# Kernel optimization log

Measured on AMD Instinct MI355X. Metric: run time of the kernel, lower is better.

The kernel has to match this reference:

```python
import jax, jax.numpy as jnp
import numpy as np

CODEBOOK_SIZE = 8192
TOKEN_SIZE = 256
COMMITMENT_COST = 0.25
B, C, H, W = 32, 256, 32, 32


def setup_inputs() -> dict:
    key = jax.random.key(0)
    k1, k2 = jax.random.split(key)
    z = jax.random.normal(k1, (B, C, H, W), dtype=jnp.float32)
    # torch init: uniform_(-1/codebook_size, 1/codebook_size)
    embedding = jax.random.uniform(
        k2, (CODEBOOK_SIZE, TOKEN_SIZE), dtype=jnp.float32,
        minval=-1.0 / CODEBOOK_SIZE, maxval=1.0 / CODEBOOK_SIZE)
    return {"z": z, "embedding": embedding}


def reference(z, embedding):
    # b c h w -> b h w c
    z = jnp.transpose(z.astype(jnp.float32), (0, 2, 3, 1))
    b, h, w, c = z.shape
    z_flat = z.reshape(-1, c)  # [N, c]

    # squared euclidean distances: ||z||^2 + ||e||^2 - 2 z e^T
    d = (jnp.sum(z_flat ** 2, axis=1, keepdims=True)
         + jnp.sum(embedding ** 2, axis=1)
         - 2.0 * jnp.einsum('nd,kd->nk', z_flat, embedding))  # [N, K]
    idx = jnp.argmin(d, axis=1)  # [N]

    z_q = embedding[idx].reshape(z.shape)  # [b,h,w,c]

    commitment_loss = COMMITMENT_COST * jnp.mean(
        (jax.lax.stop_gradient(z_q) - z) ** 2)
    codebook_loss = jnp.mean((z_q - jax.lax.stop_gradient(z)) ** 2)
    loss = commitment_loss + codebook_loss

    # straight-through estimator
    z_q_st = z + jax.lax.stop_gradient(z_q - z)
    z_q_out = jnp.transpose(z_q_st, (0, 3, 1, 2))  # b h w c -> b c h w

    min_encoding_indices = idx.reshape(b, h, w)
    return (z_q_out, loss, commitment_loss, codebook_loss,
            min_encoding_indices)
```

## Files before the change

kernel.cpp:

```cpp
#include <hip/hip_runtime.h>
#include <float.h>

#define NBATCH 32
#define NCHAN  256
#define NHW    1024
#define NTOK   32768
#define NK     8192
#define ND     256
#define ZELEMS 8388608
#define OUT_LOSS 8388608
#define OUT_IDX  8388611
#define MARGIN   1.2e-4f

typedef short bf16x8  __attribute__((ext_vector_type(8)));
typedef float f32x4   __attribute__((ext_vector_type(4)));
typedef float f32x16  __attribute__((ext_vector_type(16)));

__device__ __forceinline__ unsigned short f2bf(float f) {
    unsigned int u = __float_as_uint(f);
    u += 0x7FFFu + ((u >> 16) & 1u);
    return (unsigned short)(u >> 16);
}

__device__ __forceinline__ float embed8(float x, int code) {
    return __int_as_float((__float_as_int(x) & 0xFFFFFF00) | code);
}


__global__ __launch_bounds__(256) void k_cast(const float* __restrict__ zg,
                                              const float* __restrict__ E,
                                              unsigned short* __restrict__ Epre,
                                              unsigned short* __restrict__ Zpre,
                                              float* __restrict__ en,
                                              double* __restrict__ acc,
                                              int* __restrict__ counter) {
    __shared__ unsigned short buf[128][34];
    const int t = threadIdx.x;
    if (blockIdx.x < 1024) {
        int g = blockIdx.x * 256 + t;
        int code = g >> 5, c16 = g & 31;
        int kc = c16 >> 2, ks = (c16 >> 1) & 1, lhi = c16 & 1;
        const float4* E4 = (const float4*)(E + code * ND + c16 * 8);
        float4 a = E4[0], b = E4[1];
        float s = a.x*a.x + a.y*a.y + a.z*a.z + a.w*a.w
                + b.x*b.x + b.y*b.y + b.z*b.z + b.w*b.w;
        #pragma unroll
        for (int off = 1; off < 32; off <<= 1) s += __shfl_xor(s, off, 64);
        if ((t & 31) == 0) en[code] = s;
        unsigned int u[4];
        u[0] = (unsigned int)f2bf(a.x) | ((unsigned int)f2bf(a.y) << 16);
        u[1] = (unsigned int)f2bf(a.z) | ((unsigned int)f2bf(a.w) << 16);
        u[2] = (unsigned int)f2bf(b.x) | ((unsigned int)f2bf(b.y) << 16);
        u[3] = (unsigned int)f2bf(b.z) | ((unsigned int)f2bf(b.w) << 16);
        *(uint4*)((char*)Epre + (size_t)(code >> 7) * 65536 + kc * 8192
                  + (ks * 2 + lhi) * 2048 + (code & 127) * 16) =
            make_uint4(u[0], u[1], u[2], u[3]);
        if (blockIdx.x == 0 && t == 0) { acc[0] = 0.0; counter[0] = 0; }
    } else {
        int bi = blockIdx.x - 1024;
        int b = bi >> 6, kc = (bi >> 3) & 7, hwt = bi & 7;
        int c0 = kc * 32, hw0 = hwt * 128;
        #pragma unroll
        for (int r = 0; r < 4; ++r) {
            int idx = r * 256 + t;
            int c = idx >> 5, q = idx & 31;
            float4 v = *(const float4*)&zg[(b * 256 + c0 + c) * 1024 + hw0 + q * 4];
            buf[q * 4 + 0][c] = f2bf(v.x);
            buf[q * 4 + 1][c] = f2bf(v.y);
            buf[q * 4 + 2][c] = f2bf(v.z);
            buf[q * 4 + 3][c] = f2bf(v.w);
        }
        __syncthreads();
        int tok = t >> 1, ks = t & 1;
        char* base = (char*)Zpre + (size_t)((b * 8 + hwt) * 8 + kc) * 8192;
        #pragma unroll
        for (int lhi = 0; lhi < 2; ++lhi) {
            unsigned int u[4];
            #pragma unroll
            for (int k = 0; k < 4; ++k) {
                int cc = ks * 16 + lhi * 8 + 2 * k;
                u[k] = (unsigned int)buf[tok][cc] | ((unsigned int)buf[tok][cc + 1] << 16);
            }
            *(uint4*)(base + (ks * 2 + lhi) * 2048 + tok * 16) =
                make_uint4(u[0], u[1], u[2], u[3]);
        }
    }
}

__global__ __launch_bounds__(256, 2) void k_dist(const unsigned short* __restrict__ Epre,
                                                 const unsigned short* __restrict__ Zpre,
                                                 const float* __restrict__ en,
                                                 float2* __restrict__ part2) {
    __shared__ __align__(16) char Elds[3][16384];
    __shared__ __align__(16) char Zlds[3][8192];
    __shared__ float2 red[2][128];
    __shared__ float en_s[256];

    const int t    = threadIdx.x;
    const int kbb2 = blockIdx.x;
    const int mb   = blockIdx.y;
    const int n0   = mb * 128;
    const int w    = t >> 6, lane = t & 63;
    const int l31  = lane & 31, lhi = lane >> 5;
    const int wm   = w >> 1, wn = w & 1;

    const char* Esrc = (const char*)Epre + (size_t)kbb2 * 131072;
    const char* Zsrc = (const char*)Zpre + (size_t)mb * 65536;

    auto STAGE = [&](int bb, int kc) {
        #pragma unroll
        for (int s2 = 0; s2 < 2; ++s2)
            #pragma unroll
            for (int h = 0; h < 2; ++h)
                __builtin_amdgcn_global_load_lds(
                    (const unsigned int*)(Esrc + (size_t)s2 * 65536 + kc * 8192 + h * 4096 + t * 16),
                    (unsigned int*)&Elds[bb][s2 * 8192 + h * 4096 + t * 16], 16, 0, 0);
        #pragma unroll
        for (int h = 0; h < 2; ++h)
            __builtin_amdgcn_global_load_lds(
                (const unsigned int*)(Zsrc + kc * 8192 + h * 4096 + t * 16),
                (unsigned int*)&Zlds[bb][h * 4096 + t * 16], 16, 0, 0);
    };

    f32x16 acc[4][2];
    #pragma unroll
    for (int i = 0; i < 4; ++i)
        #pragma unroll
        for (int j = 0; j < 2; ++j) acc[i][j] = (f32x16)0.0f;

    float en_v = en[kbb2 * 256 + t];
    STAGE(0, 0);
    STAGE(1, 1);
    asm volatile("s_waitcnt vmcnt(6)" ::: "memory");
    __builtin_amdgcn_s_barrier();

    const int eoff = wm * 8192 + lhi * 2048 + l31 * 16;
    const int zoff = lhi * 2048 + (wn * 64 + l31) * 16;

    #pragma unroll
    for (int kc = 0; kc < 8; ++kc) {
        const int pp = kc % 3;
        const char* Eb = &Elds[pp][0] + eoff;
        const char* Zb = &Zlds[pp][0] + zoff;
        bf16x8 ea[4][2], zb[2][2];
        #pragma unroll
        for (int i = 0; i < 4; ++i)
            #pragma unroll
            for (int ks = 0; ks < 2; ++ks)
                ea[i][ks] = *(const bf16x8*)(Eb + ks * 4096 + i * 512);
        #pragma unroll
        for (int j = 0; j < 2; ++j)
            #pragma unroll
            for (int ks = 0; ks < 2; ++ks)
                zb[j][ks] = *(const bf16x8*)(Zb + ks * 4096 + j * 512);
        asm volatile("s_waitcnt lgkmcnt(0)" ::: "memory");
        __builtin_amdgcn_s_barrier();
        __builtin_amdgcn_sched_barrier(0);
        if (kc < 6) STAGE((kc + 2) % 3, kc + 2);

        __builtin_amdgcn_s_setprio(1);
        #pragma unroll
        for (int ks = 0; ks < 2; ++ks)
            #pragma unroll
            for (int i = 0; i < 4; ++i)
                #pragma unroll
                for (int j = 0; j < 2; ++j)
                    acc[i][j] = __builtin_amdgcn_mfma_f32_32x32x16_bf16(
                        ea[i][ks], zb[j][ks], acc[i][j], 0, 0, 0);
        __builtin_amdgcn_s_setprio(0);
        if (kc < 6)      { asm volatile("s_waitcnt vmcnt(6)" ::: "memory"); __builtin_amdgcn_s_barrier(); }
        else if (kc == 6){ asm volatile("s_waitcnt vmcnt(0)" ::: "memory"); __builtin_amdgcn_s_barrier(); }
    }

    en_s[t] = en_v;
    __syncthreads();

    float v1[2][4], v2[2][4];
    #pragma unroll
    for (int j = 0; j < 2; ++j)
        #pragma unroll
        for (int i = 0; i < 4; ++i) { v1[j][i] = FLT_MAX; v2[j][i] = FLT_MAX; }
    #pragma unroll
    for (int i = 0; i < 4; ++i) {
        const int cb = wm * 128 + i * 32 + lhi * 4;
        #pragma unroll
        for (int rq = 0; rq < 4; ++rq) {
            f32x4 ev = *(const f32x4*)&en_s[cb + 8 * rq];
            #pragma unroll
            for (int rr = 0; rr < 4; ++rr) {
                const int r = rq * 4 + rr;
                const int code = cb + 8 * rq + rr;
                #pragma unroll
                for (int j = 0; j < 2; ++j) {
                    float s  = fmaf(-2.0f, acc[i][j][r], ev[rr]);
                    float se = embed8(s, code);
                    v2[j][i] = __builtin_amdgcn_fmed3f(se, v1[j][i], v2[j][i]);
                    v1[j][i] = fminf(v1[j][i], se);
                }
            }
        }
    }
    float m1[2], m2[2];
    #pragma unroll
    for (int j = 0; j < 2; ++j) {
        float a1 = fminf(v1[j][0], v1[j][1]);
        float ah = fmaxf(v1[j][0], v1[j][1]);
        float a2 = fminf(ah, fminf(v2[j][0], v2[j][1]));
        float b1 = fminf(v1[j][2], v1[j][3]);
        float bh = fmaxf(v1[j][2], v1[j][3]);
        float b2 = fminf(bh, fminf(v2[j][2], v2[j][3]));
        m1[j] = fminf(a1, b1);
        m2[j] = fminf(fmaxf(a1, b1), fminf(a2, b2));
    }
    #pragma unroll
    for (int j = 0; j < 2; ++j) {
        float b1 = __shfl_xor(m1[j], 32, 64);
        float b2 = __shfl_xor(m2[j], 32, 64);
        float hi = fmaxf(m1[j], b1);
        m1[j] = fminf(m1[j], b1);
        m2[j] = fminf(fminf(hi, m2[j]), b2);
    }
    if (lane < 32) {
        #pragma unroll
        for (int j = 0; j < 2; ++j)
            red[wm][wn * 64 + j * 32 + l31] = make_float2(m1[j], m2[j]);
    }
    __syncthreads();
    if (t < 128) {
        float2 A = red[0][t], B = red[1][t];
        float g1 = fminf(A.x, B.x);
        float g2 = fminf(fminf(fmaxf(A.x, B.x), A.y), B.y);
        part2[(size_t)kbb2 * NTOK + n0 + t] = make_float2(g1, g2);
    }
}

__global__ __launch_bounds__(256) void k_refine(const float* __restrict__ zg,
                                                const float* __restrict__ E,
                                                const float* __restrict__ en,
                                                const float2* __restrict__ part2,
                                                int* __restrict__ idxw,
                                                float* __restrict__ outF,
                                                double* __restrict__ acc,
                                                int* __restrict__ counter) {
    __shared__ float Zs[256 * 65];
    __shared__ double lred[4];
    const int t = threadIdx.x;
    const int n0 = blockIdx.x * 64;
    const int b = n0 >> 10, hw0 = n0 & 1023;

    #pragma unroll
    for (int r = 0; r < 16; ++r) {
        int li = r * 256 + t;
        int c = li >> 4, q = li & 15;
        float4 v = *(const float4*)&zg[(b * 256 + c) * 1024 + hw0 + q * 4];
        Zs[c * 65 + q * 4 + 0] = v.x;
        Zs[c * 65 + q * 4 + 1] = v.y;
        Zs[c * 65 + q * 4 + 2] = v.z;
        Zs[c * 65 + q * 4 + 3] = v.w;
    }
    __syncthreads();

    const int w = t >> 6, l = t & 63;
    double lsum = 0.0;
    for (int it = 0; it < 16; ++it) {
        const int tokl = w * 16 + it;
        const int n = n0 + tokl;

        float zreg[4];
        #pragma unroll
        for (int j = 0; j < 4; ++j) zreg[j] = Zs[(64 * j + l) * 65 + tokl];

        double z2 = 0.0;
        #pragma unroll
        for (int j = 0; j < 4; ++j) z2 += (double)zreg[j] * (double)zreg[j];
        #pragma unroll
        for (int m = 1; m < 64; m <<= 1) z2 += __shfl_xor(z2, m, 64);
        const float z2f = (float)z2;

        float2 p = make_float2(FLT_MAX, FLT_MAX);
        if (l < 32) p = part2[(size_t)l * NTOK + n];
        int code1 = (l << 8) | (__float_as_int(p.x) & 0xFF);
        int code2 = (l << 8) | (__float_as_int(p.y) & 0xFF);

        float vmin = p.x;
        #pragma unroll
        for (int m = 1; m < 64; m <<= 1) vmin = fminf(vmin, __shfl_xor(vmin, m, 64));
        const float thr = vmin + MARGIN;

        unsigned long long m1 = __ballot(p.x <= thr);
        unsigned long long m2 = __ballot(p.y <= thr);

        float bdq = FLT_MAX; int bidx = 0x7fffffff; double gw = 0.0;
        #pragma unroll
        for (int pass = 0; pass < 2; ++pass) {
            unsigned long long mm = pass ? m2 : m1;
            int ibits = pass ? code2 : code1;
            while (mm) {
                int src = __ffsll(mm) - 1; mm &= mm - 1;
                int cidx = __shfl(ibits, src, 64);
                const float* erow = E + cidx * ND;
                double g = (double)zreg[0] * (double)erow[l]
                         + (double)zreg[1] * (double)erow[64 + l]
                         + (double)zreg[2] * (double)erow[128 + l]
                         + (double)zreg[3] * (double)erow[192 + l];
                #pragma unroll
                for (int mk = 1; mk < 64; mk <<= 1) g += __shfl_xor(g, mk, 64);
                float c  = (float)(2.0 * g);
                float dq = z2f - c;
                if (dq < bdq || (dq == bdq && cidx < bidx)) { bdq = dq; bidx = cidx; gw = g; }
            }
        }
        if (l == 0) {
            idxw[n] = bidx; outF[OUT_IDX + n] = (float)bidx;
            lsum += (double)en[bidx] - 2.0 * gw + z2;
        }
    }
    if (l == 0) lred[w] = lsum;
    __syncthreads();
    if (t == 0) {
        atomicAdd(acc, lred[0] + lred[1] + lred[2] + lred[3]);
        __threadfence();
        int old = atomicAdd(counter, 1);
        if (old == 511) {
            double total = atomicAdd(acc, 0.0);
            double mse = total / 8388608.0;
            outF[OUT_LOSS + 0] = (float)(1.25 * mse);
            outF[OUT_LOSS + 1] = (float)(0.25 * mse);
            outF[OUT_LOSS + 2] = (float)mse;
        }
    }
}

__global__ __launch_bounds__(256) void k_gather(const float* __restrict__ E,
                                                const int* __restrict__ idxw,
                                                float* __restrict__ out) {
    __shared__ __align__(16) float Es[64 * 256];
    __shared__ int sidx[64];
    const int t = threadIdx.x;
    const int b = blockIdx.x >> 4, ht = blockIdx.x & 15;

    if (t < 64) sidx[t] = idxw[b * 1024 + ht * 64 + t];
    __syncthreads();
    const float4* E4 = (const float4*)E;
    #pragma unroll
    for (int r = 0; r < 16; ++r) {
        int li = r * 256 + t;
        int row = li >> 6, slot = li & 63;
        float4 v = E4[(size_t)sidx[row] * 64 + slot];
        *(float4*)&Es[row * 256 + ((slot ^ (row & 15)) * 4)] = v;
    }
    __syncthreads();

    const int hw = t & 63, wv = t >> 6;
    #pragma unroll 8
    for (int cc = 0; cc < 64; ++cc) {
        int c = wv * 64 + cc;
        float e = Es[hw * 256 + (((c >> 2) ^ (hw & 15)) * 4) + (c & 3)];
        size_t gi = (size_t)(b * 256 + c) * 1024 + ht * 64 + hw;
        out[gi] = e;
    }
}

extern "C" void kernel_launch(void* const* d_in, const int* in_sizes, int n_in,
                              void* d_out, int out_size, void* d_ws, size_t ws_size,
                              hipStream_t stream) {
    const float* zg = (const float*)d_in[0];
    const float* E  = (const float*)d_in[1];
    float* out = (float*)d_out;
    float* wsf = (float*)d_ws;
    double* acc     = (double*)wsf;
    int*    counter = (int*)(wsf + 2);
    float*  en      = wsf + 64;
    int*    idxw    = (int*)(wsf + 64 + NK);
    float2* part2   = (float2*)(wsf + 64 + NK + NTOK);
    unsigned short* Epre = (unsigned short*)(wsf + 64 + NK + NTOK + 4194304);
    unsigned short* Zpre = (unsigned short*)d_out;

    k_cast  <<<3072, 256, 0, stream>>>(zg, E, Epre, Zpre, en, acc, counter);
    k_dist  <<<dim3(32, 256), 256, 0, stream>>>(Epre, Zpre, en, part2);
    k_refine<<<NTOK / 64, 256, 0, stream>>>(zg, E, en, part2, idxw, out, acc, counter);
    k_gather<<<512, 256, 0, stream>>>(E, idxw, out);
}
```

Before: 282.1 us.

## Load Z operand directly into double-buffered registers instead of LDS staging

```diff
diff --git a/kernel.cpp b/kernel.cpp
--- a/kernel.cpp
+++ b/kernel.cpp
@@ -92,7 +92,6 @@
                                                  const float* __restrict__ en,
                                                  float2* __restrict__ part2) {
     __shared__ __align__(16) char Elds[3][16384];
-    __shared__ __align__(16) char Zlds[3][8192];
     __shared__ float2 red[2][128];
     __shared__ float en_s[256];
 
@@ -107,7 +106,7 @@
     const char* Esrc = (const char*)Epre + (size_t)kbb2 * 131072;
     const char* Zsrc = (const char*)Zpre + (size_t)mb * 65536;
 
-    auto STAGE = [&](int bb, int kc) {
+    auto STAGE_E = [&](int bb, int kc) {
         #pragma unroll
         for (int s2 = 0; s2 < 2; ++s2)
             #pragma unroll
@@ -115,13 +114,19 @@
                 __builtin_amdgcn_global_load_lds(
                     (const unsigned int*)(Esrc + (size_t)s2 * 65536 + kc * 8192 + h * 4096 + t * 16),
                     (unsigned int*)&Elds[bb][s2 * 8192 + h * 4096 + t * 16], 16, 0, 0);
-        #pragma unroll
-        for (int h = 0; h < 2; ++h)
-            __builtin_amdgcn_global_load_lds(
-                (const unsigned int*)(Zsrc + kc * 8192 + h * 4096 + t * 16),
-                (unsigned int*)&Zlds[bb][h * 4096 + t * 16], 16, 0, 0);
     };
 
+    bf16x8 zbR[2][2][2];
+    const char* Zp = Zsrc + lhi * 2048 + (wn * 64 + l31) * 16;
+    auto LOADZ = [&](int set, int kc) {
+        const char* p = Zp + kc * 8192;
+        #pragma unroll
+        for (int j = 0; j < 2; ++j)
+            #pragma unroll
+            for (int ks = 0; ks < 2; ++ks)
+                zbR[set][j][ks] = *(const bf16x8*)(p + ks * 4096 + j * 512);
+    };
+
     f32x16 acc[4][2];
     #pragma unroll
     for (int i = 0; i < 4; ++i)
@@ -129,34 +134,30 @@
         for (int j = 0; j < 2; ++j) acc[i][j] = (f32x16)0.0f;
 
     float en_v = en[kbb2 * 256 + t];
-    STAGE(0, 0);
-    STAGE(1, 1);
-    asm volatile("s_waitcnt vmcnt(6)" ::: "memory");
+    LOADZ(0, 0);
+    STAGE_E(0, 0);
+    STAGE_E(1, 1);
+    asm volatile("s_waitcnt vmcnt(4)" ::: "memory");
     __builtin_amdgcn_s_barrier();
 
     const int eoff = wm * 8192 + lhi * 2048 + l31 * 16;
-    const int zoff = lhi * 2048 + (wn * 64 + l31) * 16;
 
     #pragma unroll
     for (int kc = 0; kc < 8; ++kc) {
-        const int pp = kc % 3;
-        const char* Eb = &Elds[pp][0] + eoff;
-        const char* Zb = &Zlds[pp][0] + zoff;
-        bf16x8 ea[4][2], zb[2][2];
+        const int eb = kc % 3, zs = kc & 1;
+        const char* Eb = &Elds[eb][0] + eoff;
+        bf16x8 ea[4][2];
         #pragma unroll
         for (int i = 0; i < 4; ++i)
             #pragma unroll
             for (int ks = 0; ks < 2; ++ks)
                 ea[i][ks] = *(const bf16x8*)(Eb + ks * 4096 + i * 512);
-        #pragma unroll
-        for (int j = 0; j < 2; ++j)
-            #pragma unroll
-            for (int ks = 0; ks < 2; ++ks)
-                zb[j][ks] = *(const bf16x8*)(Zb + ks * 4096 + j * 512);
         asm volatile("s_waitcnt lgkmcnt(0)" ::: "memory");
         __builtin_amdgcn_s_barrier();
         __builtin_amdgcn_sched_barrier(0);
-        if (kc < 6) STAGE((kc + 2) % 3, kc + 2);
+        if (kc < 7) LOADZ(zs ^ 1, kc + 1);
+        __builtin_amdgcn_sched_barrier(0);
+        if (kc < 6) STAGE_E((kc + 2) % 3, kc + 2);
 
         __builtin_amdgcn_s_setprio(1);
         #pragma unroll
@@ -166,9 +167,9 @@
                 #pragma unroll
                 for (int j = 0; j < 2; ++j)
                     acc[i][j] = __builtin_amdgcn_mfma_f32_32x32x16_bf16(
-                        ea[i][ks], zb[j][ks], acc[i][j], 0, 0, 0);
+                        ea[i][ks], zbR[zs][j][ks], acc[i][j], 0, 0, 0);
         __builtin_amdgcn_s_setprio(0);
-        if (kc < 6)      { asm volatile("s_waitcnt vmcnt(6)" ::: "memory"); __builtin_amdgcn_s_barrier(); }
+        if (kc < 6)      { asm volatile("s_waitcnt vmcnt(4)" ::: "memory"); __builtin_amdgcn_s_barrier(); }
         else if (kc == 6){ asm volatile("s_waitcnt vmcnt(0)" ::: "memory"); __builtin_amdgcn_s_barrier(); }
     }
 
```

Result: slower. 290.0 us (+2.8%).
